# Kernel tuning notes

Hardware: AMD Instinct MI355X
Metric: run time of the kernel (lower is better)

The kernel has to match this reference:

```python
import jax, jax.numpy as jnp
import numpy as np

HEADS = 16
DIM_HEAD = 64
LN_EPS = 1e-3  # keras LayerNormalization default


def setup_inputs() -> dict:
    key = jax.random.key(0)
    ks = jax.random.split(key, 4)
    B, N, D = 8, 512, 1024
    inner = HEADS * DIM_HEAD  # 1024
    return {
        "x": jax.random.normal(ks[0], (B, N, D), dtype=jnp.float32),
        "w_qkv": jax.random.normal(ks[1], (D, 3 * inner), dtype=jnp.float32) * (D ** -0.5),
        "reattn_w": jax.random.normal(ks[2], (HEADS, HEADS), dtype=jnp.float32),
        "ln_gamma": jnp.ones((HEADS,), dtype=jnp.float32),
        "ln_beta": jnp.zeros((HEADS,), dtype=jnp.float32),
        "w_out": jax.random.normal(ks[3], (inner, D), dtype=jnp.float32) * (inner ** -0.5),
        "b_out": jnp.zeros((D,), dtype=jnp.float32),
    }


def reference(x, w_qkv, reattn_w, ln_gamma, ln_beta, w_out, b_out):
    B, N, D = x.shape
    H, dh = HEADS, DIM_HEAD
    scale = dh ** -0.5

    qkv = x @ w_qkv  # [B, N, 3*H*dh]
    q, k, v = jnp.split(qkv, 3, axis=-1)
    # b n (h d) -> b h n d
    to_heads = lambda t: t.reshape(B, N, H, dh).transpose(0, 2, 1, 3)
    q, k, v = to_heads(q), to_heads(k), to_heads(v)

    dots = jnp.einsum("bhid,bhjd->bhij", q, k) * scale  # [B, H, N, N]
    attn = jax.nn.softmax(dots, axis=-1)

    # re-attention: mix across heads
    attn = jnp.einsum("bhij,hg->bgij", attn, reattn_w)

    # LayerNorm over the head axis (axis=1), keras default eps
    mean = jnp.mean(attn, axis=1, keepdims=True)
    var = jnp.var(attn, axis=1, keepdims=True)
    attn = (attn - mean) * jax.lax.rsqrt(var + LN_EPS)
    attn = attn * ln_gamma[None, :, None, None] + ln_beta[None, :, None, None]

    out = jnp.einsum("bhij,bhjd->bhid", attn, v)  # [B, H, N, dh]
    out = out.transpose(0, 2, 1, 3).reshape(B, N, H * dh)  # b h n d -> b n (h d)
    return out @ w_out + b_out
```

## Files before the change

### kernel.cpp

```cpp
#include <hip/hip_runtime.h>
#include <math.h>

#define BB 8
#define NN 512
#define DD 1024
#define HH 16
#define DH 64
#define INNER 1024
#define QKV3 3072
#define PSTR (NN * NN + 64)

typedef __attribute__((ext_vector_type(8))) short short8;
typedef __attribute__((ext_vector_type(4))) float f32x4;

#define AS1 __attribute__((address_space(1)))
#define AS3 __attribute__((address_space(3)))

__device__ __forceinline__ float4 ld4(const float* p) { return *(const float4*)p; }

__device__ __forceinline__ unsigned short f2bf(float f) {
    unsigned u = __float_as_uint(f);
    return (unsigned short)((u + 0x7fffu + ((u >> 16) & 1u)) >> 16);
}
__device__ __forceinline__ float bf2f(unsigned short u) {
    return __uint_as_float(((unsigned)u) << 16);
}

__global__ void conv_bf16(const float* __restrict__ in, unsigned short* __restrict__ out) {
    size_t i = ((size_t)blockIdx.x * 256 + threadIdx.x) * 4;
    float4 v = ld4(in + i);
    ushort4 o;
    o.x = f2bf(v.x); o.y = f2bf(v.y); o.z = f2bf(v.z); o.w = f2bf(v.w);
    *(ushort4*)(out + i) = o;
}

__global__ void convT_bf16(const float* __restrict__ in, unsigned short* __restrict__ out,
                           int K, int N) {
    __shared__ float t[32][33];
    const int n0 = blockIdx.x * 32, k0 = blockIdx.y * 32;
    const int tx = threadIdx.x & 31, ty = threadIdx.x >> 5;
#pragma unroll
    for (int l = 0; l < 4; ++l)
        t[ty + 8 * l][tx] = in[(size_t)(k0 + ty + 8 * l) * N + n0 + tx];
    __syncthreads();
#pragma unroll
    for (int l = 0; l < 4; ++l)
        out[(size_t)(n0 + ty + 8 * l) * K + k0 + tx] = f2bf(t[tx][ty + 8 * l]);
}

__global__ __launch_bounds__(256) void gemm_bf16(
    const unsigned short* __restrict__ A, const unsigned short* __restrict__ Bt,
    float* __restrict__ C, const float* __restrict__ bias, int M, int N, int K) {
    __shared__ short As[128 * 32];
    __shared__ short Bs[128 * 32];
    const int tid = threadIdx.x;
    const int w = tid >> 6, l = tid & 63;
    const int bm = blockIdx.y * 128, bn = blockIdx.x * 128;
    const int wm = (w >> 1) * 64, wn = (w & 1) * 64;
    const int lrow = l & 15, lq = l >> 4;

    f32x4 acc[4][4];
#pragma unroll
    for (int i = 0; i < 4; ++i)
#pragma unroll
        for (int j = 0; j < 4; ++j) acc[i][j] = (f32x4){0.f, 0.f, 0.f, 0.f};

    for (int k0 = 0; k0 < K; k0 += 32) {
#pragma unroll
        for (int t = 0; t < 2; ++t) {
            const int q = w * 2 + t;
            const int li = q * 512 + l * 8;
            const int row = li >> 5, kc = li & 31;
            const unsigned short* ga = A + (size_t)(bm + row) * K + k0 + kc;
            __builtin_amdgcn_global_load_lds(
                (const AS1 void*)ga, (AS3 void*)(As + q * 512), 16, 0, 0);
            const unsigned short* gb = Bt + (size_t)(bn + row) * K + k0 + kc;
            __builtin_amdgcn_global_load_lds(
                (const AS1 void*)gb, (AS3 void*)(Bs + q * 512), 16, 0, 0);
        }
        __syncthreads();

        short8 a[4], b[4];
#pragma unroll
        for (int i = 0; i < 4; ++i)
            a[i] = *(const short8*)(As + (wm + i * 16 + lrow) * 32 + lq * 8);
#pragma unroll
        for (int j = 0; j < 4; ++j)
            b[j] = *(const short8*)(Bs + (wn + j * 16 + lrow) * 32 + lq * 8);
#pragma unroll
        for (int i = 0; i < 4; ++i)
#pragma unroll
            for (int j = 0; j < 4; ++j)
                acc[i][j] = __builtin_amdgcn_mfma_f32_16x16x32_bf16(a[i], b[j], acc[i][j], 0, 0, 0);
        __syncthreads();
    }

#pragma unroll
    for (int i = 0; i < 4; ++i)
#pragma unroll
        for (int j = 0; j < 4; ++j) {
            const int col = bn + wn + j * 16 + lrow;
            const float bv = bias ? bias[col] : 0.f;
#pragma unroll
            for (int r = 0; r < 4; ++r) {
                const int row = bm + wm + i * 16 + lq * 4 + r;
                C[(size_t)row * N + col] = acc[i][j][r] + bv;
            }
        }
}

__device__ __forceinline__ void stage_st(const unsigned short* __restrict__ G, int K,
                                         int row0, int kt, short* dst_half,
                                         int w, int l) {
    const int grow = row0 + w * 16 + (l >> 2);
    const int gcol = kt * 32 + (((l & 3) * 8) ^ ((l & 32) ? 16 : 0));
    __builtin_amdgcn_global_load_lds(
        (const AS1 void*)(G + (size_t)grow * K + gcol),
        (AS3 void*)(dst_half + w * 512), 16, 0, 0);
}

__global__ __launch_bounds__(512, 2) void gemm256_bf(
    const unsigned short* __restrict__ A, const unsigned short* __restrict__ Bt,
    unsigned short* __restrict__ C, int M, int N, int K) {
    __shared__ __align__(16) short lds_[2 * 16384];
    const int tid = threadIdx.x;
    const int w = tid >> 6, l = tid & 63;
    const int wm = w >> 2, wn = w & 3;
    const int lrow = l & 15, lq = l >> 4;
    const int bm = blockIdx.y * 256, bn = blockIdx.x * 256;
    const int NT = K >> 5;

    const int aoff = lrow * 32 + ((lq * 8) ^ ((lrow & 8) ? 16 : 0));
    const int bsub = (wn & 1) * 4;

    f32x4 acc[8][4];
#pragma unroll
    for (int i = 0; i < 8; ++i)
#pragma unroll
        for (int j = 0; j < 4; ++j) acc[i][j] = (f32x4){0.f, 0.f, 0.f, 0.f};

    stage_st(A,  K, bm,       0, lds_ + 0,                    w, l);
    stage_st(A,  K, bm + 128, 0, lds_ + 4096,                 w, l);
    stage_st(Bt, K, bn,       0, lds_ + 8192,                 w, l);
    stage_st(Bt, K, bn + 128, 0, lds_ + 8192 + 4096,          w, l);
    stage_st(Bt, K, bn,       1, lds_ + 16384 + 8192,         w, l);
    stage_st(Bt, K, bn + 128, 1, lds_ + 16384 + 8192 + 4096,  w, l);
    asm volatile("s_waitcnt vmcnt(2)" ::: "memory");
    __builtin_amdgcn_s_barrier();

    for (int t = 0; t < NT; ++t) {
        const int s = t & 1;
        const short* Ah = lds_ + s * 16384 + wm * 4096;
        const short* Bh = lds_ + s * 16384 + 8192 + (wn >> 1) * 4096;
        short8 bfr[4];
#pragma unroll
        for (int p = 0; p < 4; ++p) {
            short8 a0 = *(const short8*)(Ah + (2 * p) * 512 + aoff);
            short8 a1 = *(const short8*)(Ah + (2 * p + 1) * 512 + aoff);
            if (p == 0) {
#pragma unroll
                for (int fc = 0; fc < 4; ++fc)
                    bfr[fc] = *(const short8*)(Bh + (bsub + fc) * 512 + aoff);
            }
            if (p == 0 && t + 1 < NT)
                stage_st(A,  K, bm,       t + 1, lds_ + (s ^ 1) * 16384,               w, l);
            if (p == 1 && t + 1 < NT)
                stage_st(A,  K, bm + 128, t + 1, lds_ + (s ^ 1) * 16384 + 4096,        w, l);
            if (p == 2 && t + 2 < NT)
                stage_st(Bt, K, bn,       t + 2, lds_ + s * 16384 + 8192,              w, l);
            if (p == 3 && t + 2 < NT)
                stage_st(Bt, K, bn + 128, t + 2, lds_ + s * 16384 + 8192 + 4096,       w, l);

            __builtin_amdgcn_s_barrier();
            asm volatile("s_waitcnt lgkmcnt(0)" ::: "memory");
            __builtin_amdgcn_sched_barrier(0);

            __builtin_amdgcn_s_setprio(1);
#pragma unroll
            for (int fc = 0; fc < 4; ++fc) {
                acc[2 * p][fc] =
                    __builtin_amdgcn_mfma_f32_16x16x32_bf16(a0, bfr[fc], acc[2 * p][fc], 0, 0, 0);
                acc[2 * p + 1][fc] =
                    __builtin_amdgcn_mfma_f32_16x16x32_bf16(a1, bfr[fc], acc[2 * p + 1][fc], 0, 0, 0);
            }
            __builtin_amdgcn_s_setprio(0);

            if (p == 3) {
                if (t == NT - 2)
                    asm volatile("s_waitcnt vmcnt(0)" ::: "memory");
                else if (t < NT - 2)
                    asm volatile("s_waitcnt vmcnt(2)" ::: "memory");
            }
            __builtin_amdgcn_s_barrier();
        }
    }

#pragma unroll
    for (int fr = 0; fr < 8; ++fr)
#pragma unroll
        for (int fc = 0; fc < 4; ++fc) {
            const int col = bn + wn * 64 + fc * 16 + lrow;
#pragma unroll
            for (int r = 0; r < 4; ++r) {
                const int row = bm + wm * 128 + fr * 16 + lq * 4 + r;
                C[(size_t)row * N + col] = f2bf(acc[fr][fc][r]);
            }
        }
}

__global__ __launch_bounds__(256) void scores_stream(
    const unsigned short* __restrict__ qkvb, unsigned short* __restrict__ attnb,
    float* __restrict__ lsum2) {
    __shared__ unsigned short obuf[4][16][264];
    const int bh = blockIdx.x;
    const int h = bh & 15, b = bh >> 4;
    const int jh = blockIdx.y;
    const int w = threadIdx.x >> 6, l = threadIdx.x & 63;
    const int i0 = blockIdx.z * 64 + w * 16;
    const int lrow = l & 15, lq = l >> 4;

    const unsigned short* qb = qkvb + (size_t)(b * NN) * QKV3 + h * DH + lq * 8;
    const unsigned short* kb = qkvb + (size_t)(b * NN) * QKV3 + INNER + h * DH + lq * 8;

    const short8 qf0 = *(const short8*)(qb + (size_t)(i0 + lrow) * QKV3);
    const short8 qf1 = *(const short8*)(qb + (size_t)(i0 + lrow) * QKV3 + 32);

    const unsigned short* krow = kb + (size_t)(jh * 256 + lrow) * QKV3;

    short8 ka[4], kc[4];
#pragma unroll
    for (int p = 0; p < 4; ++p) {
        const unsigned short* kp = krow + (size_t)p * 16 * QKV3;
        ka[p] = *(const short8*)(kp);
        kc[p] = *(const short8*)(kp + 32);
    }

    float lacc = 0.f;
#pragma unroll
    for (int jt = 0; jt < 16; ++jt) {
        const int s = jt & 3;
        short8 kf0 = ka[s], kf1 = kc[s];
        if (jt < 12) {
            const unsigned short* kp = krow + (size_t)(jt + 4) * 16 * QKV3;
            ka[s] = *(const short8*)(kp);
            kc[s] = *(const short8*)(kp + 32);
        }
        f32x4 acc = (f32x4){0.f, 0.f, 0.f, 0.f};
        acc = __builtin_amdgcn_mfma_f32_16x16x32_bf16(kf0, qf0, acc, 0, 0, 0);
        acc = __builtin_amdgcn_mfma_f32_16x16x32_bf16(kf1, qf1, acc, 0, 0, 0);
        float e0 = __expf(acc[0] * 0.125f);
        float e1 = __expf(acc[1] * 0.125f);
        float e2 = __expf(acc[2] * 0.125f);
        float e3 = __expf(acc[3] * 0.125f);
        lacc += (e0 + e1) + (e2 + e3);
        ushort4 o;
        o.x = f2bf(e0); o.y = f2bf(e1); o.z = f2bf(e2); o.w = f2bf(e3);
        *(ushort4*)(&obuf[w][lrow][jt * 16 + lq * 4]) = o;
    }
    lacc += __shfl_xor(lacc, 16, 64);
    lacc += __shfl_xor(lacc, 32, 64);
    if (lq == 0)
        lsum2[(size_t)jh * BB * HH * NN + (size_t)bh * NN + i0 + lrow] = lacc;

    unsigned short* obase = attnb + (size_t)bh * PSTR + (size_t)i0 * NN + jh * 256;
#pragma unroll
    for (int r = 0; r < 16; ++r)
        *(ushort4*)(obase + (size_t)r * NN + l * 4) =
            *(const ushort4*)(&obuf[w][r][l * 4]);
}

__global__ void reattn_ln_bf(unsigned short* __restrict__ attnb,
                             const float* __restrict__ lsum2,
                             const float* __restrict__ rw,
                             const float* __restrict__ gamma,
                             const float* __restrict__ beta) {
    __shared__ float w[16][16];
    __shared__ float gs[16], bs[16];
    const int tid = threadIdx.x;
    ((float*)w)[tid] = rw[tid];
    if (tid < 16) { gs[tid] = gamma[tid]; bs[tid] = beta[tid]; }
    __syncthreads();

    const size_t idx = (size_t)blockIdx.x * 256 + tid;
    const int j4 = (int)(idx & 127);
    const int i = (int)((idx >> 7) & 511);
    const int b = (int)(idx >> 16);
    unsigned short* base = attnb + (size_t)(b * HH) * PSTR + (size_t)i * NN + j4 * 4;
    const float* l0 = lsum2 + (size_t)(b * HH) * NN + i;
    const float* l1 = l0 + (size_t)BB * HH * NN;

    float v[16][4];
#pragma unroll
    for (int h = 0; h < 16; ++h) {
        const float linv = 1.0f / (l0[h * NN] + l1[h * NN]);
        ushort4 u = *(const ushort4*)(base + (size_t)h * PSTR);
        v[h][0] = bf2f(u.x) * linv; v[h][1] = bf2f(u.y) * linv;
        v[h][2] = bf2f(u.z) * linv; v[h][3] = bf2f(u.w) * linv;
    }
    float o[16][4];
    float me[4] = {0.f, 0.f, 0.f, 0.f};
#pragma unroll
    for (int g = 0; g < 16; ++g) {
        float s0 = 0.f, s1 = 0.f, s2 = 0.f, s3 = 0.f;
#pragma unroll
        for (int h = 0; h < 16; ++h) {
            const float wg = w[h][g];
            s0 += v[h][0] * wg; s1 += v[h][1] * wg;
            s2 += v[h][2] * wg; s3 += v[h][3] * wg;
        }
        o[g][0] = s0; o[g][1] = s1; o[g][2] = s2; o[g][3] = s3;
        me[0] += s0; me[1] += s1; me[2] += s2; me[3] += s3;
    }
#pragma unroll
    for (int r = 0; r < 4; ++r) me[r] *= 0.0625f;
    float va[4] = {0.f, 0.f, 0.f, 0.f};
#pragma unroll
    for (int g = 0; g < 16; ++g)
#pragma unroll
        for (int r = 0; r < 4; ++r) {
            float d = o[g][r] - me[r];
            va[r] += d * d;
        }
    float ri[4];
#pragma unroll
    for (int r = 0; r < 4; ++r) ri[r] = rsqrtf(va[r] * 0.0625f + 1e-3f);
#pragma unroll
    for (int g = 0; g < 16; ++g) {
        ushort4 u;
        u.x = f2bf((o[g][0] - me[0]) * ri[0] * gs[g] + bs[g]);
        u.y = f2bf((o[g][1] - me[1]) * ri[1] * gs[g] + bs[g]);
        u.z = f2bf((o[g][2] - me[2]) * ri[2] * gs[g] + bs[g]);
        u.w = f2bf((o[g][3] - me[3]) * ri[3] * gs[g] + bs[g]);
        *(ushort4*)(base + (size_t)g * PSTR) = u;
    }
}

__global__ void transpose_v(const unsigned short* __restrict__ qkvb,
                            unsigned short* __restrict__ vT) {
    __shared__ unsigned short t[32][33];
    const int bh = blockIdx.z;
    const int h = bh & 15, b = bh >> 4;
    const int j0 = blockIdx.x * 32, d0 = blockIdx.y * 32;
    const int tx = threadIdx.x & 31, ty = threadIdx.x >> 5;
    const unsigned short* src = qkvb + (size_t)(b * NN) * QKV3 + 2 * INNER + h * DH;
#pragma unroll
    for (int k = 0; k < 4; ++k)
        t[ty + 8 * k][tx] = src[(size_t)(j0 + ty + 8 * k) * QKV3 + d0 + tx];
    __syncthreads();
    unsigned short* dst = vT + (size_t)bh * DH * NN;
#pragma unroll
    for (int k = 0; k < 4; ++k)
        dst[(size_t)(d0 + ty + 8 * k) * NN + j0 + tx] = t[tx][ty + 8 * k];
}

__global__ __launch_bounds__(256) void pv_mfma(
    const unsigned short* __restrict__ attnb, const unsigned short* __restrict__ vT,
    unsigned short* __restrict__ outhb) {
    const int bh = blockIdx.x;
    const int h = bh & 15, b = bh >> 4;
    const int i0 = blockIdx.y * 128;
    __shared__ short Ps[128 * 64];
    __shared__ short Vs[64 * 64];
    const int tid = threadIdx.x;
    const int w = tid >> 6, l = tid & 63;
    const int lrow = l & 15, lq = l >> 4;
    const int lr8 = l >> 3;
    const int swd = ((l & 7) ^ (lr8 & 7)) * 8;

    f32x4 acc[2][4];
#pragma unroll
    for (int ic = 0; ic < 2; ++ic)
#pragma unroll
        for (int dt = 0; dt < 4; ++dt) acc[ic][dt] = (f32x4){0.f, 0.f, 0.f, 0.f};

    const unsigned short* pb = attnb + (size_t)bh * PSTR + (size_t)i0 * NN;
    const unsigned short* vb = vT + (size_t)bh * DH * NN;

    for (int j0 = 0; j0 < NN; j0 += 64) {
#pragma unroll
        for (int t = 0; t < 4; ++t) {
            int c = w * 4 + t;
            int r = c * 8 + lr8;
            __builtin_amdgcn_global_load_lds(
                (const AS1 void*)(pb + (size_t)r * NN + j0 + swd),
                (AS3 void*)(Ps + c * 512), 16, 0, 0);
        }
#pragma unroll
        for (int t = 0; t < 2; ++t) {
            int c = w * 2 + t;
            int d = c * 8 + lr8;
            __builtin_amdgcn_global_load_lds(
                (const AS1 void*)(vb + (size_t)d * NN + j0 + swd),
                (AS3 void*)(Vs + c * 512), 16, 0, 0);
        }
        __syncthreads();

#pragma unroll
        for (int kh = 0; kh < 2; ++kh) {
            short8 vf[4];
#pragma unroll
            for (int dt = 0; dt < 4; ++dt)
                vf[dt] = *(const short8*)(Vs + (dt * 16 + lrow) * 64 + (((kh * 4 + lq) ^ (lrow & 7)) * 8));
#pragma unroll
            for (int ic = 0; ic < 2; ++ic) {
                short8 pf = *(const short8*)(Ps + (w * 32 + ic * 16 + lrow) * 64 + (((kh * 4 + lq) ^ (lrow & 7)) * 8));
#pragma unroll
                for (int dt = 0; dt < 4; ++dt)
                    acc[ic][dt] = __builtin_amdgcn_mfma_f32_16x16x32_bf16(vf[dt], pf, acc[ic][dt], 0, 0, 0);
            }
        }
        __syncthreads();
    }

#pragma unroll
    for (int ic = 0; ic < 2; ++ic) {
        unsigned short* orow = outhb +
            ((size_t)(b * NN + i0 + w * 32 + ic * 16 + lrow)) * INNER + h * DH + lq * 4;
#pragma unroll
        for (int dt = 0; dt < 4; ++dt) {
            ushort4 o;
            o.x = f2bf(acc[ic][dt][0]); o.y = f2bf(acc[ic][dt][1]);
            o.z = f2bf(acc[ic][dt][2]); o.w = f2bf(acc[ic][dt][3]);
            *(ushort4*)(orow + dt * 16) = o;
        }
    }
}

extern "C" void kernel_launch(void* const* d_in, const int* in_sizes, int n_in,
                              void* d_out, int out_size, void* d_ws, size_t ws_size,
                              hipStream_t stream) {
    const float* x        = (const float*)d_in[0];
    const float* w_qkv    = (const float*)d_in[1];
    const float* reattn_w = (const float*)d_in[2];
    const float* ln_gamma = (const float*)d_in[3];
    const float* ln_beta  = (const float*)d_in[4];
    const float* w_out    = (const float*)d_in[5];
    const float* b_out    = (const float*)d_in[6];
    float* out = (float*)d_out;

    unsigned short* qkvb  = (unsigned short*)d_ws;
    unsigned short* attnb = qkvb + (size_t)BB * NN * QKV3;
    unsigned short* vTb   = attnb + (size_t)BB * HH * PSTR;
    unsigned short* outhb = vTb + (size_t)BB * HH * DH * NN;
    unsigned short* xb    = outhb + (size_t)BB * NN * INNER;
    unsigned short* wqkvT = xb + (size_t)BB * NN * DD;
    unsigned short* woutT = wqkvT + (size_t)DD * QKV3;
    float*          lsum2 = (float*)(woutT + (size_t)INNER * INNER);

    dim3 blk(256);

    conv_bf16<<<dim3((BB * NN * DD) / 1024), blk, 0, stream>>>(x, xb);
    convT_bf16<<<dim3(QKV3 / 32, DD / 32), blk, 0, stream>>>(w_qkv, wqkvT, DD, QKV3);
    convT_bf16<<<dim3(INNER / 32, INNER / 32), blk, 0, stream>>>(w_out, woutT, INNER, INNER);

    gemm256_bf<<<dim3(QKV3 / 256, (BB * NN) / 256), dim3(512), 0, stream>>>(
        xb, wqkvT, qkvb, BB * NN, QKV3, DD);

    scores_stream<<<dim3(BB * HH, 2, NN / 64), blk, 0, stream>>>(qkvb, attnb, lsum2);

    reattn_ln_bf<<<dim3((BB * NN * NN) / 1024), blk, 0, stream>>>(
        attnb, lsum2, reattn_w, ln_gamma, ln_beta);

    transpose_v<<<dim3(NN / 32, DH / 32, BB * HH), blk, 0, stream>>>(qkvb, vTb);

    pv_mfma<<<dim3(BB * HH, NN / 128), blk, 0, stream>>>(attnb, vTb, outhb);

    gemm_bf16<<<dim3(INNER / 128, (BB * NN) / 128), blk, 0, stream>>>(
        outhb, woutT, out, b_out, BB * NN, INNER, INNER);
}
```

Baseline: 236.3 us.

## Simplify GEMM double-buffer pipeline and stage K tile in LDS for scores

The bf16 GEMM main loop drops the interleaved per-quarter prefetch with split A/B staging and multiple barriers. It now uses a plain double buffer: issue all next-tile loads, read all fragments, run 32 MFMAs, then wait on vmcnt(0) and one barrier. The scores kernel now loads its 256x64 K tile once into swizzled LDS via global_load_lds instead of per-wave register prefetch from global, which removes redundant K reads across the four waves. It also shrinks the output staging buffer and writes results in 64-column chunks. The trade-offs are less overlap of global loads with compute in the GEMM and a block-wide barrier before scoring.

After: 219.2 us. -7.2%, faster.

```diff
diff --git a/kernel.cpp b/kernel.cpp
--- a/kernel.cpp
+++ b/kernel.cpp
@@ -139,60 +139,45 @@
 #pragma unroll
         for (int j = 0; j < 4; ++j) acc[i][j] = (f32x4){0.f, 0.f, 0.f, 0.f};
 
-    stage_st(A,  K, bm,       0, lds_ + 0,                    w, l);
-    stage_st(A,  K, bm + 128, 0, lds_ + 4096,                 w, l);
-    stage_st(Bt, K, bn,       0, lds_ + 8192,                 w, l);
-    stage_st(Bt, K, bn + 128, 0, lds_ + 8192 + 4096,          w, l);
-    stage_st(Bt, K, bn,       1, lds_ + 16384 + 8192,         w, l);
-    stage_st(Bt, K, bn + 128, 1, lds_ + 16384 + 8192 + 4096,  w, l);
-    asm volatile("s_waitcnt vmcnt(2)" ::: "memory");
+    stage_st(A,  K, bm,       0, lds_ + 0,     w, l);
+    stage_st(A,  K, bm + 128, 0, lds_ + 4096,  w, l);
+    stage_st(Bt, K, bn,       0, lds_ + 8192,  w, l);
+    stage_st(Bt, K, bn + 128, 0, lds_ + 12288, w, l);
+    asm volatile("s_waitcnt vmcnt(0)" ::: "memory");
     __builtin_amdgcn_s_barrier();
 
     for (int t = 0; t < NT; ++t) {
         const int s = t & 1;
+        if (t + 1 < NT) {
+            short* nb = lds_ + (s ^ 1) * 16384;
+            stage_st(A,  K, bm,       t + 1, nb,         w, l);
+            stage_st(A,  K, bm + 128, t + 1, nb + 4096,  w, l);
+            stage_st(Bt, K, bn,       t + 1, nb + 8192,  w, l);
+            stage_st(Bt, K, bn + 128, t + 1, nb + 12288, w, l);
+        }
         const short* Ah = lds_ + s * 16384 + wm * 4096;
         const short* Bh = lds_ + s * 16384 + 8192 + (wn >> 1) * 4096;
-        short8 bfr[4];
-#pragma unroll
-        for (int p = 0; p < 4; ++p) {
-            short8 a0 = *(const short8*)(Ah + (2 * p) * 512 + aoff);
-            short8 a1 = *(const short8*)(Ah + (2 * p + 1) * 512 + aoff);
-            if (p == 0) {
-#pragma unroll
-                for (int fc = 0; fc < 4; ++fc)
-                    bfr[fc] = *(const short8*)(Bh + (bsub + fc) * 512 + aoff);
-            }
-            if (p == 0 && t + 1 < NT)
-                stage_st(A,  K, bm,       t + 1, lds_ + (s ^ 1) * 16384,               w, l);
-            if (p == 1 && t + 1 < NT)
-                stage_st(A,  K, bm + 128, t + 1, lds_ + (s ^ 1) * 16384 + 4096,        w, l);
-            if (p == 2 && t + 2 < NT)
-                stage_st(Bt, K, bn,       t + 2, lds_ + s * 16384 + 8192,              w, l);
-            if (p == 3 && t + 2 < NT)
-                stage_st(Bt, K, bn + 128, t + 2, lds_ + s * 16384 + 8192 + 4096,       w, l);
-
-            __builtin_amdgcn_s_barrier();
-            asm volatile("s_waitcnt lgkmcnt(0)" ::: "memory");
-            __builtin_amdgcn_sched_barrier(0);
-
-            __builtin_amdgcn_s_setprio(1);
-#pragma unroll
-            for (int fc = 0; fc < 4; ++fc) {
-                acc[2 * p][fc] =
-                    __builtin_amdgcn_mfma_f32_16x16x32_bf16(a0, bfr[fc], acc[2 * p][fc], 0, 0, 0);
-                acc[2 * p + 1][fc] =
-                    __builtin_amdgcn_mfma_f32_16x16x32_bf16(a1, bfr[fc], acc[2 * p + 1][fc], 0, 0, 0);
-            }
-            __builtin_amdgcn_s_setprio(0);
-
-            if (p == 3) {
-                if (t == NT - 2)
-                    asm volatile("s_waitcnt vmcnt(0)" ::: "memory");
-                else if (t < NT - 2)
-                    asm volatile("s_waitcnt vmcnt(2)" ::: "memory");
-            }
-            __builtin_amdgcn_s_barrier();
-        }
+        short8 a[8], bfr[4];
+#pragma unroll
+        for (int i = 0; i < 8; ++i)
+            a[i] = *(const short8*)(Ah + i * 512 + aoff);
+#pragma unroll
+        for (int j = 0; j < 4; ++j)
+            bfr[j] = *(const short8*)(Bh + (bsub + j) * 512 + aoff);
+
+        asm volatile("s_waitcnt lgkmcnt(0)" ::: "memory");
+        __builtin_amdgcn_sched_barrier(0);
+
+        __builtin_amdgcn_s_setprio(1);
+#pragma unroll
+        for (int i = 0; i < 8; ++i)
+#pragma unroll
+            for (int j = 0; j < 4; ++j)
+                acc[i][j] = __builtin_amdgcn_mfma_f32_16x16x32_bf16(a[i], bfr[j], acc[i][j], 0, 0, 0);
+        __builtin_amdgcn_s_setprio(0);
+
+        asm volatile("s_waitcnt vmcnt(0)" ::: "memory");
+        __builtin_amdgcn_s_barrier();
     }
 
 #pragma unroll
@@ -211,7 +196,8 @@
 __global__ __launch_bounds__(256) void scores_stream(
     const unsigned short* __restrict__ qkvb, unsigned short* __restrict__ attnb,
     float* __restrict__ lsum2) {
-    __shared__ unsigned short obuf[4][16][264];
+    __shared__ unsigned short Ks[256 * 64];
+    __shared__ unsigned short obuf[4][16][68];
     const int bh = blockIdx.x;
     const int h = bh & 15, b = bh >> 4;
     const int jh = blockIdx.y;
@@ -219,32 +205,32 @@
     const int i0 = blockIdx.z * 64 + w * 16;
     const int lrow = l & 15, lq = l >> 4;
 
+    const unsigned short* kbase =
+        qkvb + (size_t)(b * NN + jh * 256) * QKV3 + INNER + h * DH;
+#pragma unroll
+    for (int i = 0; i < 8; ++i) {
+        const int r = (w * 8 + i) * 8 + (l >> 3);
+        const int c = (l & 7) ^ (r & 7);
+        __builtin_amdgcn_global_load_lds(
+            (const AS1 void*)(kbase + (size_t)r * QKV3 + c * 8),
+            (AS3 void*)(Ks + (w * 8 + i) * 512), 16, 0, 0);
+    }
+
     const unsigned short* qb = qkvb + (size_t)(b * NN) * QKV3 + h * DH + lq * 8;
-    const unsigned short* kb = qkvb + (size_t)(b * NN) * QKV3 + INNER + h * DH + lq * 8;
-
     const short8 qf0 = *(const short8*)(qb + (size_t)(i0 + lrow) * QKV3);
     const short8 qf1 = *(const short8*)(qb + (size_t)(i0 + lrow) * QKV3 + 32);
 
-    const unsigned short* krow = kb + (size_t)(jh * 256 + lrow) * QKV3;
-
-    short8 ka[4], kc[4];
-#pragma unroll
-    for (int p = 0; p < 4; ++p) {
-        const unsigned short* kp = krow + (size_t)p * 16 * QKV3;
-        ka[p] = *(const short8*)(kp);
-        kc[p] = *(const short8*)(kp + 32);
-    }
-
+    asm volatile("s_waitcnt vmcnt(0)" ::: "memory");
+    __syncthreads();
+
+    unsigned short* obase = attnb + (size_t)bh * PSTR + (size_t)i0 * NN + jh * 256;
+    const int sw = lrow & 7;
     float lacc = 0.f;
 #pragma unroll
     for (int jt = 0; jt < 16; ++jt) {
-        const int s = jt & 3;
-        short8 kf0 = ka[s], kf1 = kc[s];
-        if (jt < 12) {
-            const unsigned short* kp = krow + (size_t)(jt + 4) * 16 * QKV3;
-            ka[s] = *(const short8*)(kp);
-            kc[s] = *(const short8*)(kp + 32);
-        }
+        const int R = jt * 16 + lrow;
+        const short8 kf0 = *(const short8*)(Ks + R * 64 + ((lq ^ sw) * 8));
+        const short8 kf1 = *(const short8*)(Ks + R * 64 + (((4 + lq) ^ sw) * 8));
         f32x4 acc = (f32x4){0.f, 0.f, 0.f, 0.f};
         acc = __builtin_amdgcn_mfma_f32_16x16x32_bf16(kf0, qf0, acc, 0, 0, 0);
         acc = __builtin_amdgcn_mfma_f32_16x16x32_bf16(kf1, qf1, acc, 0, 0, 0);
@@ -255,18 +241,22 @@
         lacc += (e0 + e1) + (e2 + e3);
         ushort4 o;
         o.x = f2bf(e0); o.y = f2bf(e1); o.z = f2bf(e2); o.w = f2bf(e3);
-        *(ushort4*)(&obuf[w][lrow][jt * 16 + lq * 4]) = o;
+        *(ushort4*)(&obuf[w][lrow][(jt & 3) * 16 + lq * 4]) = o;
+        if ((jt & 3) == 3) {
+            const int jb = (jt >> 2) * 64;
+#pragma unroll
+            for (int q = 0; q < 4; ++q) {
+                const int rr = q * 4 + (l >> 4);
+                const int cc = l & 15;
+                *(ushort4*)(obase + (size_t)rr * NN + jb + cc * 4) =
+                    *(const ushort4*)(&obuf[w][rr][cc * 4]);
+            }
+        }
     }
     lacc += __shfl_xor(lacc, 16, 64);
     lacc += __shfl_xor(lacc, 32, 64);
     if (lq == 0)
         lsum2[(size_t)jh * BB * HH * NN + (size_t)bh * NN + i0 + lrow] = lacc;
-
-    unsigned short* obase = attnb + (size_t)bh * PSTR + (size_t)i0 * NN + jh * 256;
-#pragma unroll
-    for (int r = 0; r < 16; ++r)
-        *(ushort4*)(obase + (size_t)r * NN + l * 4) =
-            *(const ushort4*)(&obuf[w][r][l * 4]);
 }
 
 __global__ void reattn_ln_bf(unsigned short* __restrict__ attnb,
```
